# Kernel optimization log

Hardware: AMD Instinct MI355X
Metric: run time of the kernel (lower is better)

## Reference

```python
import jax, jax.numpy as jnp
import numpy as np

EPS = 1e-5
L, S, B, IN, H = 2, 256, 128, 256, 256  # num_layers, seq_len, batch, input_size, hidden_size


def _ln(v):
    # LayerNorm over last dim (4H), no affine (affine applied by caller)
    m = jnp.mean(v, axis=-1, keepdims=True)
    var = jnp.mean(jnp.square(v - m), axis=-1, keepdims=True)
    return (v - m) * jax.lax.rsqrt(var + EPS)


def setup_inputs() -> dict:
    key = jax.random.key(0)
    ks = jax.random.split(key, 8)
    gain = float(np.sqrt(1.0 / H))
    x = jax.random.normal(ks[0], (S, B, IN), dtype=jnp.float32)
    h0 = jax.random.normal(ks[1], (L, B, H), dtype=jnp.float32)
    c0 = jax.random.normal(ks[2], (L, B, H), dtype=jnp.float32)
    wx = jax.random.uniform(ks[3], (L, IN, 4 * H), jnp.float32, -gain, gain)
    wh = jax.random.uniform(ks[4], (L, H, 4 * H), jnp.float32, -gain, gain)
    bias = jax.random.uniform(ks[5], (L, 4 * H), jnp.float32, -gain, gain)
    ln_gamma = jnp.ones((L, 8 * H), dtype=jnp.float32)
    ln_beta = jnp.zeros((L, 8 * H), dtype=jnp.float32)
    return {"x": x, "h0": h0, "c0": c0, "wx": wx, "wh": wh, "bias": bias,
            "ln_gamma": ln_gamma, "ln_beta": ln_beta}


def lstm_forward(x, h0, c0, wx, wh, bias, ln_gamma, ln_beta):
    hs, cs = [], []
    for l in range(L):
        gx_gamma, gh_gamma = ln_gamma[l, :4 * H], ln_gamma[l, 4 * H:]
        gx_beta, gh_beta = ln_beta[l, :4 * H], ln_beta[l, 4 * H:]
        # input contribution for all timesteps at once: [S, B, 4H]
        gx = _ln(jnp.einsum('sbi,ig->sbg', x, wx[l])) * gx_gamma + gx_beta
        wh_l, b_l = wh[l], bias[l]

        def step(carry, gx_t):
            h, c = carry
            gh = _ln(h @ wh_l) * gh_gamma + gh_beta
            gate = gx_t + gh + b_l
            i, f, o, g = jnp.split(gate, 4, axis=-1)
            i = jax.nn.sigmoid(i)
            f = jax.nn.sigmoid(f)
            o = jax.nn.sigmoid(o)
            g = jnp.tanh(g)
            c_new = f * c + i * g
            h_new = o * jnp.tanh(c_new)
            return (h_new, c_new), h_new

        (hT, cT), ys = jax.lax.scan(step, (h0[l], c0[l]), gx)
        x = ys  # dropout = 0.0 -> identity between layers
        hs.append(hT)
        cs.append(cT)
    return x, jnp.stack(hs, 0), jnp.stack(cs, 0)


def reference(x, h0, c0, wx, wh, bias, ln_gamma, ln_beta):
    # Returns (output [S,B,H], h_n [L,B,H], c_n [L,B,H])
    return lstm_forward(x, h0, c0, wx, wh, bias, ln_gamma, ln_beta)
```

## Files before the change

### kernel.cpp

```cpp
#include <hip/hip_runtime.h>
#include <math.h>

#define SS   256
#define BB   128
#define INN  256
#define HH   256
#define NG   1024
#define NL   2
#define EPSV 1e-5f

__device__ __forceinline__ float sum4(float4 v)   { return v.x + v.y + v.z + v.w; }
__device__ __forceinline__ float sumsq4(float4 v) { return v.x*v.x + v.y*v.y + v.z*v.z + v.w*v.w; }
__device__ __forceinline__ float fast_sigmoid(float x) { return 1.0f / (1.0f + __expf(-x)); }
__device__ __forceinline__ float fast_tanh(float x) {
  float t = __expf(-2.0f * fabsf(x));
  float r = (1.0f - t) / (1.0f + t);
  return copysignf(r, x);
}

__global__ void init_state(const float* __restrict__ h0, const float* __restrict__ c0,
                           float* __restrict__ hs, float* __restrict__ cs, int n) {
  int i = blockIdx.x * blockDim.x + threadIdx.x;
  if (i < n) { hs[i] = h0[i]; cs[i] = c0[i]; }
}

__global__ __launch_bounds__(256) void gemm_gx(const float* __restrict__ A,
                                               const float* __restrict__ W,
                                               float* __restrict__ C) {
  __shared__ __align__(16) float As[16][132];
  __shared__ __align__(16) float Bs[16][132];
  const int tid = threadIdx.x;
  const int bn  = blockIdx.x * 128;
  const int bm  = blockIdx.y * 128;
  const int tx  = tid & 15;
  const int ty  = tid >> 4;
  const int am  = tid >> 1;
  const int ac  = (tid & 1) << 3;
  const int br  = tid >> 4;
  const int bc  = (tid & 15) << 2;

  float acc[8][8] = {};
  for (int k0 = 0; k0 < INN; k0 += 16) {
    const float4 a0 = *(const float4*)&A[(size_t)(bm + am) * INN + k0 + ac];
    const float4 a1 = *(const float4*)&A[(size_t)(bm + am) * INN + k0 + ac + 4];
    const float4 b0 = *(const float4*)&W[(size_t)(k0 + br) * NG + bn + bc];
    const float4 b1 = *(const float4*)&W[(size_t)(k0 + br) * NG + bn + bc + 64];
    __syncthreads();
    As[ac + 0][am] = a0.x; As[ac + 1][am] = a0.y; As[ac + 2][am] = a0.z; As[ac + 3][am] = a0.w;
    As[ac + 4][am] = a1.x; As[ac + 5][am] = a1.y; As[ac + 6][am] = a1.z; As[ac + 7][am] = a1.w;
    *(float4*)&Bs[br][bc]      = b0;
    *(float4*)&Bs[br][bc + 64] = b1;
    __syncthreads();
#pragma unroll
    for (int k = 0; k < 16; ++k) {
      const float4 av0 = *(const float4*)&As[k][ty << 3];
      const float4 av1 = *(const float4*)&As[k][(ty << 3) + 4];
      const float4 bv0 = *(const float4*)&Bs[k][tx << 3];
      const float4 bv1 = *(const float4*)&Bs[k][(tx << 3) + 4];
      const float a[8] = {av0.x, av0.y, av0.z, av0.w, av1.x, av1.y, av1.z, av1.w};
      const float b[8] = {bv0.x, bv0.y, bv0.z, bv0.w, bv1.x, bv1.y, bv1.z, bv1.w};
#pragma unroll
      for (int i = 0; i < 8; ++i)
#pragma unroll
        for (int j = 0; j < 8; ++j) acc[i][j] += a[i] * b[j];
    }
  }
#pragma unroll
  for (int i = 0; i < 8; ++i) {
    const size_t row = (size_t)(bm + (ty << 3) + i) * NG + bn + (tx << 3);
    float4 o0 = {acc[i][0], acc[i][1], acc[i][2], acc[i][3]};
    float4 o1 = {acc[i][4], acc[i][5], acc[i][6], acc[i][7]};
    *(float4*)&C[row]     = o0;
    *(float4*)&C[row + 4] = o1;
  }
}

__global__ __launch_bounds__(256) void lstm_rec(
    const float* __restrict__ gx,
    const float* __restrict__ whl,
    float* __restrict__ hsl,
    float* __restrict__ csl,
    const float* __restrict__ gam,
    const float* __restrict__ bet,
    const float* __restrict__ bias,
    float* __restrict__ ys,
    int t0, int nsteps)
{
  __shared__ __align__(16) float hbuf[2][HH];
  __shared__ __align__(16) float gex[2][NG];
  __shared__ float red[4][8];

  const int tid = threadIdx.x;
  const int b0  = blockIdx.x * 2;
  const int lane = tid & 63;
  const int wid  = tid >> 6;

  const float4 gxg = *(const float4*)&gam[4 * tid];
  const float4 gxb = *(const float4*)&bet[4 * tid];
  const float4 ghg = *(const float4*)&gam[NG + 4 * tid];
  const float4 ghb = *(const float4*)&bet[NG + 4 * tid];
  const float4 bi  = *(const float4*)&bias[4 * tid];

  float c[2];
  c[0] = csl[(b0 + 0) * HH + tid];
  c[1] = csl[(b0 + 1) * HH + tid];
  hbuf[0][tid] = hsl[(b0 + 0) * HH + tid];
  hbuf[1][tid] = hsl[(b0 + 1) * HH + tid];
  __syncthreads();

  const float4* wh4 = (const float4*)whl;

  for (int t = 0; t < nsteps; ++t) {
    const float4 x0 = *(const float4*)&gx[((size_t)t * BB + b0 + 0) * NG + 4 * tid];
    const float4 x1 = *(const float4*)&gx[((size_t)t * BB + b0 + 1) * NG + 4 * tid];

    float4 a0 = {0, 0, 0, 0}, a1 = {0, 0, 0, 0};
#pragma unroll 8
    for (int k = 0; k < HH; k += 4) {
      float4 hv0 = *(const float4*)&hbuf[0][k];
      float4 hv1 = *(const float4*)&hbuf[1][k];
      float h0a[4] = {hv0.x, hv0.y, hv0.z, hv0.w};
      float h1a[4] = {hv1.x, hv1.y, hv1.z, hv1.w};
#pragma unroll
      for (int kk = 0; kk < 4; ++kk) {
        float4 w = wh4[(k + kk) * (NG / 4) + tid];
        a0.x += h0a[kk] * w.x; a0.y += h0a[kk] * w.y;
        a0.z += h0a[kk] * w.z; a0.w += h0a[kk] * w.w;
        a1.x += h1a[kk] * w.x; a1.y += h1a[kk] * w.y;
        a1.z += h1a[kk] * w.z; a1.w += h1a[kk] * w.w;
      }
    }

    float v[8] = {sum4(a0), sumsq4(a0), sum4(a1), sumsq4(a1),
                  sum4(x0), sumsq4(x0), sum4(x1), sumsq4(x1)};
#pragma unroll
    for (int off = 32; off; off >>= 1)
#pragma unroll
      for (int j = 0; j < 8; ++j) v[j] += __shfl_xor(v[j], off);
    if (lane == 0) {
#pragma unroll
      for (int j = 0; j < 8; ++j) red[wid][j] = v[j];
    }
    __syncthreads();
    float s[8];
#pragma unroll
    for (int j = 0; j < 8; ++j)
      s[j] = red[0][j] + red[1][j] + red[2][j] + red[3][j];

    const float inv = 1.0f / (float)NG;
    const float muh0 = s[0] * inv, muh1 = s[2] * inv;
    const float mux0 = s[4] * inv, mux1 = s[6] * inv;
    const float rsh0 = rsqrtf(s[1] * inv - muh0 * muh0 + EPSV);
    const float rsh1 = rsqrtf(s[3] * inv - muh1 * muh1 + EPSV);
    const float rsx0 = rsqrtf(s[5] * inv - mux0 * mux0 + EPSV);
    const float rsx1 = rsqrtf(s[7] * inv - mux1 * mux1 + EPSV);

    float4 g0, g1;
    g0.x = (x0.x - mux0) * rsx0 * gxg.x + gxb.x + (a0.x - muh0) * rsh0 * ghg.x + ghb.x + bi.x;
    g0.y = (x0.y - mux0) * rsx0 * gxg.y + gxb.y + (a0.y - muh0) * rsh0 * ghg.y + ghb.y + bi.y;
    g0.z = (x0.z - mux0) * rsx0 * gxg.z + gxb.z + (a0.z - muh0) * rsh0 * ghg.z + ghb.z + bi.z;
    g0.w = (x0.w - mux0) * rsx0 * gxg.w + gxb.w + (a0.w - muh0) * rsh0 * ghg.w + ghb.w + bi.w;
    g1.x = (x1.x - mux1) * rsx1 * gxg.x + gxb.x + (a1.x - muh1) * rsh1 * ghg.x + ghb.x + bi.x;
    g1.y = (x1.y - mux1) * rsx1 * gxg.y + gxb.y + (a1.y - muh1) * rsh1 * ghg.y + ghb.y + bi.y;
    g1.z = (x1.z - mux1) * rsx1 * gxg.z + gxb.z + (a1.z - muh1) * rsh1 * ghg.z + ghb.z + bi.z;
    g1.w = (x1.w - mux1) * rsx1 * gxg.w + gxb.w + (a1.w - muh1) * rsh1 * ghg.w + ghb.w + bi.w;

    *(float4*)&gex[0][4 * tid] = g0;
    *(float4*)&gex[1][4 * tid] = g1;
    __syncthreads();

#pragma unroll
    for (int r = 0; r < 2; ++r) {
      const float gi = gex[r][tid];
      const float gf = gex[r][256 + tid];
      const float go = gex[r][512 + tid];
      const float gg = gex[r][768 + tid];
      const float ii = fast_sigmoid(gi);
      const float ff = fast_sigmoid(gf);
      const float oo = fast_sigmoid(go);
      const float g  = fast_tanh(gg);
      const float cn = ff * c[r] + ii * g;
      const float hn = oo * fast_tanh(cn);
      c[r] = cn;
      hbuf[r][tid] = hn;
      ys[((size_t)(t0 + t) * BB + b0 + r) * HH + tid] = hn;
    }
    __syncthreads();
  }

  hsl[(b0 + 0) * HH + tid] = hbuf[0][tid];
  hsl[(b0 + 1) * HH + tid] = hbuf[1][tid];
  csl[(b0 + 0) * HH + tid] = c[0];
  csl[(b0 + 1) * HH + tid] = c[1];
}

extern "C" void kernel_launch(void* const* d_in, const int* in_sizes, int n_in,
                              void* d_out, int out_size, void* d_ws, size_t ws_size,
                              hipStream_t stream) {
  const float* x    = (const float*)d_in[0];
  const float* h0   = (const float*)d_in[1];
  const float* c0   = (const float*)d_in[2];
  const float* wx   = (const float*)d_in[3];
  const float* wh   = (const float*)d_in[4];
  const float* bias = (const float*)d_in[5];
  const float* gam  = (const float*)d_in[6];
  const float* bet  = (const float*)d_in[7];

  float* out  = (float*)d_out;
  float* ys_x = out;
  float* hs   = out + (size_t)SS * BB * HH;
  float* cs   = hs + (size_t)NL * BB * HH;
  float* gxbuf = (float*)d_ws;

  const size_t step_bytes = (size_t)BB * NG * sizeof(float);
  int T = (int)(ws_size / step_bytes);
  if (T > SS) T = SS;
  if (T < 1)  T = 1;

  const int nstate = NL * BB * HH;
  init_state<<<(nstate + 255) / 256, 256, 0, stream>>>(h0, c0, hs, cs, nstate);

  for (int l = 0; l < NL; ++l) {
    const float* Ain = (l == 0) ? x : ys_x;
    for (int t0 = 0; t0 < SS; t0 += T) {
      const int nt = (SS - t0 < T) ? (SS - t0) : T;
      const dim3 ggrid(NG / 128, nt);
      gemm_gx<<<ggrid, 256, 0, stream>>>(Ain + (size_t)t0 * BB * INN,
                                         wx + (size_t)l * INN * NG, gxbuf);
      lstm_rec<<<BB / 2, 256, 0, stream>>>(
          gxbuf, wh + (size_t)l * HH * NG,
          hs + (size_t)l * BB * HH, cs + (size_t)l * BB * HH,
          gam + (size_t)l * 2 * NG, bet + (size_t)l * 2 * NG,
          bias + (size_t)l * NG, ys_x, t0, nt);
    }
  }
}
```

Before: 12.12 ms.

## Use one batch row per block with register double-buffered Wh loads

The recurrent kernel now handles one batch row per block instead of two, launching 128 blocks rather than 64, so more CUs take part in the serial time loop. The Wh matvec loads weights in 16-row chunks into two register buffers, fetching the next chunk while the current one is consumed to hide global/L2 latency. Each block now streams the full Wh matrix per step for only one row, which doubles total weight traffic. The larger register footprint is allowed by launch_bounds(256,1).

```diff
diff --git a/kernel.cpp b/kernel.cpp
--- a/kernel.cpp
+++ b/kernel.cpp
@@ -75,7 +75,7 @@
   }
 }
 
-__global__ __launch_bounds__(256) void lstm_rec(
+__global__ __launch_bounds__(256, 1) void lstm_rec(
     const float* __restrict__ gx,
     const float* __restrict__ whl,
     float* __restrict__ hsl,
@@ -86,12 +86,12 @@
     float* __restrict__ ys,
     int t0, int nsteps)
 {
-  __shared__ __align__(16) float hbuf[2][HH];
-  __shared__ __align__(16) float gex[2][NG];
-  __shared__ float red[4][8];
+  __shared__ __align__(16) float hbuf[HH];
+  __shared__ __align__(16) float gex[NG];
+  __shared__ float red[4][4];
 
   const int tid = threadIdx.x;
-  const int b0  = blockIdx.x * 2;
+  const int b   = blockIdx.x;
   const int lane = tid & 63;
   const int wid  = tid >> 6;
 
@@ -101,97 +101,96 @@
   const float4 ghb = *(const float4*)&bet[NG + 4 * tid];
   const float4 bi  = *(const float4*)&bias[4 * tid];
 
-  float c[2];
-  c[0] = csl[(b0 + 0) * HH + tid];
-  c[1] = csl[(b0 + 1) * HH + tid];
-  hbuf[0][tid] = hsl[(b0 + 0) * HH + tid];
-  hbuf[1][tid] = hsl[(b0 + 1) * HH + tid];
+  float c = csl[b * HH + tid];
+  hbuf[tid] = hsl[b * HH + tid];
   __syncthreads();
 
-  const float4* wh4 = (const float4*)whl;
+  const float4* w4 = (const float4*)whl;
 
   for (int t = 0; t < nsteps; ++t) {
-    const float4 x0 = *(const float4*)&gx[((size_t)t * BB + b0 + 0) * NG + 4 * tid];
-    const float4 x1 = *(const float4*)&gx[((size_t)t * BB + b0 + 1) * NG + 4 * tid];
-
-    float4 a0 = {0, 0, 0, 0}, a1 = {0, 0, 0, 0};
-#pragma unroll 8
-    for (int k = 0; k < HH; k += 4) {
-      float4 hv0 = *(const float4*)&hbuf[0][k];
-      float4 hv1 = *(const float4*)&hbuf[1][k];
-      float h0a[4] = {hv0.x, hv0.y, hv0.z, hv0.w};
-      float h1a[4] = {hv1.x, hv1.y, hv1.z, hv1.w};
-#pragma unroll
-      for (int kk = 0; kk < 4; ++kk) {
-        float4 w = wh4[(k + kk) * (NG / 4) + tid];
-        a0.x += h0a[kk] * w.x; a0.y += h0a[kk] * w.y;
-        a0.z += h0a[kk] * w.z; a0.w += h0a[kk] * w.w;
-        a1.x += h1a[kk] * w.x; a1.y += h1a[kk] * w.y;
-        a1.z += h1a[kk] * w.z; a1.w += h1a[kk] * w.w;
+    const float4 x0 = *(const float4*)&gx[((size_t)t * BB + b) * NG + 4 * tid];
+
+    float4 acc = {0.f, 0.f, 0.f, 0.f};
+    float4 wA[16], wB[16];
+#pragma unroll
+    for (int j = 0; j < 16; ++j) wA[j] = w4[j * (NG / 4) + tid];
+
+#pragma unroll
+    for (int s = 0; s < 8; ++s) {
+      const int kA = s * 32;
+#pragma unroll
+      for (int j = 0; j < 16; ++j) wB[j] = w4[(kA + 16 + j) * (NG / 4) + tid];
+#pragma unroll
+      for (int j = 0; j < 16; j += 4) {
+        const float4 h4 = *(const float4*)&hbuf[kA + j];
+        acc.x += h4.x * wA[j].x + h4.y * wA[j+1].x + h4.z * wA[j+2].x + h4.w * wA[j+3].x;
+        acc.y += h4.x * wA[j].y + h4.y * wA[j+1].y + h4.z * wA[j+2].y + h4.w * wA[j+3].y;
+        acc.z += h4.x * wA[j].z + h4.y * wA[j+1].z + h4.z * wA[j+2].z + h4.w * wA[j+3].z;
+        acc.w += h4.x * wA[j].w + h4.y * wA[j+1].w + h4.z * wA[j+2].w + h4.w * wA[j+3].w;
       }
-    }
-
-    float v[8] = {sum4(a0), sumsq4(a0), sum4(a1), sumsq4(a1),
-                  sum4(x0), sumsq4(x0), sum4(x1), sumsq4(x1)};
+      if (s < 7) {
+#pragma unroll
+        for (int j = 0; j < 16; ++j) wA[j] = w4[(kA + 32 + j) * (NG / 4) + tid];
+      }
+#pragma unroll
+      for (int j = 0; j < 16; j += 4) {
+        const float4 h4 = *(const float4*)&hbuf[kA + 16 + j];
+        acc.x += h4.x * wB[j].x + h4.y * wB[j+1].x + h4.z * wB[j+2].x + h4.w * wB[j+3].x;
+        acc.y += h4.x * wB[j].y + h4.y * wB[j+1].y + h4.z * wB[j+2].y + h4.w * wB[j+3].y;
+        acc.z += h4.x * wB[j].z + h4.y * wB[j+1].z + h4.z * wB[j+2].z + h4.w * wB[j+3].z;
+        acc.w += h4.x * wB[j].w + h4.y * wB[j+1].w + h4.z * wB[j+2].w + h4.w * wB[j+3].w;
+      }
+    }
+
+    float v[4] = {sum4(acc), sumsq4(acc), sum4(x0), sumsq4(x0)};
 #pragma unroll
     for (int off = 32; off; off >>= 1)
 #pragma unroll
-      for (int j = 0; j < 8; ++j) v[j] += __shfl_xor(v[j], off);
+      for (int j = 0; j < 4; ++j) v[j] += __shfl_xor(v[j], off);
     if (lane == 0) {
 #pragma unroll
-      for (int j = 0; j < 8; ++j) red[wid][j] = v[j];
-    }
-    __syncthreads();
-    float s[8];
-#pragma unroll
-    for (int j = 0; j < 8; ++j)
-      s[j] = red[0][j] + red[1][j] + red[2][j] + red[3][j];
+      for (int j = 0; j < 4; ++j) red[wid][j] = v[j];
+    }
+    __syncthreads();
+    float s0 = red[0][0] + red[1][0] + red[2][0] + red[3][0];
+    float s1 = red[0][1] + red[1][1] + red[2][1] + red[3][1];
+    float s2 = red[0][2] + red[1][2] + red[2][2] + red[3][2];
+    float s3 = red[0][3] + red[1][3] + red[2][3] + red[3][3];
 
     const float inv = 1.0f / (float)NG;
-    const float muh0 = s[0] * inv, muh1 = s[2] * inv;
-    const float mux0 = s[4] * inv, mux1 = s[6] * inv;
-    const float rsh0 = rsqrtf(s[1] * inv - muh0 * muh0 + EPSV);
-    const float rsh1 = rsqrtf(s[3] * inv - muh1 * muh1 + EPSV);
-    const float rsx0 = rsqrtf(s[5] * inv - mux0 * mux0 + EPSV);
-    const float rsx1 = rsqrtf(s[7] * inv - mux1 * mux1 + EPSV);
-
-    float4 g0, g1;
-    g0.x = (x0.x - mux0) * rsx0 * gxg.x + gxb.x + (a0.x - muh0) * rsh0 * ghg.x + ghb.x + bi.x;
-    g0.y = (x0.y - mux0) * rsx0 * gxg.y + gxb.y + (a0.y - muh0) * rsh0 * ghg.y + ghb.y + bi.y;
-    g0.z = (x0.z - mux0) * rsx0 * gxg.z + gxb.z + (a0.z - muh0) * rsh0 * ghg.z + ghb.z + bi.z;
-    g0.w = (x0.w - mux0) * rsx0 * gxg.w + gxb.w + (a0.w - muh0) * rsh0 * ghg.w + ghb.w + bi.w;
-    g1.x = (x1.x - mux1) * rsx1 * gxg.x + gxb.x + (a1.x - muh1) * rsh1 * ghg.x + ghb.x + bi.x;
-    g1.y = (x1.y - mux1) * rsx1 * gxg.y + gxb.y + (a1.y - muh1) * rsh1 * ghg.y + ghb.y + bi.y;
-    g1.z = (x1.z - mux1) * rsx1 * gxg.z + gxb.z + (a1.z - muh1) * rsh1 * ghg.z + ghb.z + bi.z;
-    g1.w = (x1.w - mux1) * rsx1 * gxg.w + gxb.w + (a1.w - muh1) * rsh1 * ghg.w + ghb.w + bi.w;
-
-    *(float4*)&gex[0][4 * tid] = g0;
-    *(float4*)&gex[1][4 * tid] = g1;
-    __syncthreads();
-
-#pragma unroll
-    for (int r = 0; r < 2; ++r) {
-      const float gi = gex[r][tid];
-      const float gf = gex[r][256 + tid];
-      const float go = gex[r][512 + tid];
-      const float gg = gex[r][768 + tid];
+    const float muh = s0 * inv, mux = s2 * inv;
+    const float rsh = rsqrtf(s1 * inv - muh * muh + EPSV);
+    const float rsx = rsqrtf(s3 * inv - mux * mux + EPSV);
+
+    float4 g0;
+    g0.x = (x0.x - mux) * rsx * gxg.x + gxb.x + (acc.x - muh) * rsh * ghg.x + ghb.x + bi.x;
+    g0.y = (x0.y - mux) * rsx * gxg.y + gxb.y + (acc.y - muh) * rsh * ghg.y + ghb.y + bi.y;
+    g0.z = (x0.z - mux) * rsx * gxg.z + gxb.z + (acc.z - muh) * rsh * ghg.z + ghb.z + bi.z;
+    g0.w = (x0.w - mux) * rsx * gxg.w + gxb.w + (acc.w - muh) * rsh * ghg.w + ghb.w + bi.w;
+    *(float4*)&gex[4 * tid] = g0;
+    __syncthreads();
+
+    {
+      const float gi = gex[tid];
+      const float gf = gex[256 + tid];
+      const float go = gex[512 + tid];
+      const float gg = gex[768 + tid];
       const float ii = fast_sigmoid(gi);
       const float ff = fast_sigmoid(gf);
       const float oo = fast_sigmoid(go);
       const float g  = fast_tanh(gg);
-      const float cn = ff * c[r] + ii * g;
+      const float cn = ff * c + ii * g;
       const float hn = oo * fast_tanh(cn);
-      c[r] = cn;
-      hbuf[r][tid] = hn;
-      ys[((size_t)(t0 + t) * BB + b0 + r) * HH + tid] = hn;
-    }
-    __syncthreads();
-  }
-
-  hsl[(b0 + 0) * HH + tid] = hbuf[0][tid];
-  hsl[(b0 + 1) * HH + tid] = hbuf[1][tid];
-  csl[(b0 + 0) * HH + tid] = c[0];
-  csl[(b0 + 1) * HH + tid] = c[1];
+      c = cn;
+      __syncthreads();
+      hbuf[tid] = hn;
+      ys[((size_t)(t0 + t) * BB + b) * HH + tid] = hn;
+    }
+    __syncthreads();
+  }
+
+  hsl[b * HH + tid] = hbuf[tid];
+  csl[b * HH + tid] = c;
 }
 
 extern "C" void kernel_launch(void* const* d_in, const int* in_sizes, int n_in,
@@ -227,7 +226,7 @@
       const dim3 ggrid(NG / 128, nt);
       gemm_gx<<<ggrid, 256, 0, stream>>>(Ain + (size_t)t0 * BB * INN,
                                          wx + (size_t)l * INN * NG, gxbuf);
-      lstm_rec<<<BB / 2, 256, 0, stream>>>(
+      lstm_rec<<<BB, 256, 0, stream>>>(
           gxbuf, wh + (size_t)l * HH * NG,
           hs + (size_t)l * BB * HH, cs + (size_t)l * BB * HH,
           gam + (size_t)l * 2 * NG, bet + (size_t)l * 2 * NG,
```

After: 16.22 ms. 1.34x slower.
